# Kernel optimization log

Measured on AMD Instinct MI355X. Metric: run time of the kernel, lower is better.

The kernel has to match this reference:

```python
import jax, jax.numpy as jnp
import numpy as np

N_ITEMS = 512
N_SAMPLES = 32768
WINDOW = 512
CHUNK = WINDOW // 2 + 1          # 257 rfft bins
N_COEFFS = CHUNK * 3             # 771: [mags | phases | start mags]
STEP = WINDOW // 2               # 256 hop
N_FRAMES = N_SAMPLES // STEP     # 128
BASE_RES = 0.5
SPAN = 1.0 - BASE_RES
EPS = 1e-12

_HANN = jnp.asarray(np.hanning(WINDOW), dtype=jnp.float32)


def setup_inputs() -> dict:
    key = jax.random.key(0)
    k1, k2, k3 = jax.random.split(key, 3)
    selections = jax.random.normal(k1, (8, 16, 4, N_ITEMS), dtype=jnp.float32)
    # init(x): uniform(-6, 6) * bernoulli(p=0.01)  -> sparse large-magnitude coeffs
    vals = jax.random.uniform(k2, (N_ITEMS, N_COEFFS), minval=-6.0, maxval=6.0, dtype=jnp.float32)
    mask = (jax.random.uniform(k3, (N_ITEMS, N_COEFFS)) < 0.01).astype(jnp.float32)
    items = vals * mask
    return {"selections": selections, "items": items}


def _resonance_synth(coeffs):
    # coeffs: (B, E, X, N_COEFFS)
    mags = BASE_RES + jax.nn.sigmoid(coeffs[..., :CHUNK]) * 0.9999 * SPAN       # decay per frame, in (0.5, 1)
    phases = jnp.tanh(coeffs[..., CHUNK:2 * CHUNK]) * jnp.pi                    # per-frame phase advance
    starts = jax.nn.sigmoid(coeffs[..., 2 * CHUNK:])                            # initial bin magnitudes

    # log-space cumulative decay scan across frames: mag at frame t = mags ** (t+1)
    t = jnp.arange(1, N_FRAMES + 1, dtype=jnp.float32)                          # (F,)
    log_m = jnp.log(mags + EPS)                                                 # (B,E,X,C)
    decay = jnp.exp(log_m[..., None, :] * t[:, None])                           # (B,E,X,F,C)
    phi = phases[..., None, :] * t[:, None]                                     # cumulative phase rotation

    spec = (starts[..., None, :] * decay).astype(jnp.complex64) * jnp.exp(1j * phi.astype(jnp.complex64))
    frames = jnp.fft.irfft(spec, n=WINDOW, axis=-1).astype(jnp.float32)         # (B,E,X,F,W)
    frames = frames * _HANN

    first = frames[..., :STEP]                                                  # (B,E,X,F,STEP)
    second = frames[..., STEP:]
    shifted = jnp.concatenate([jnp.zeros_like(second[..., :1, :]), second[..., :-1, :]], axis=-2)
    out = first + shifted                                                       # (B,E,X,F,STEP)
    return out.reshape(*frames.shape[:-2], N_FRAMES * STEP)                     # (B,E,X,N_SAMPLES)


def reference(selections, items):
    # select_items with selection_type='relu': non-negative mixture over the item table
    selected = jnp.einsum('bexi,ic->bexc', jax.nn.relu(selections), items)      # (B,E,X,N_COEFFS)
    res = _resonance_synth(selected)                                            # (B,E,X,N_SAMPLES)
    norm = jnp.linalg.norm(res, axis=-1, keepdims=True)
    return res / (norm + 1e-8)                                                  # unit_norm along samples
```

## Files before the change

### kernel.cpp

```cpp
#include <hip/hip_runtime.h>
#include <math.h>

#define N_ROWS   512
#define NBINS    257
#define N_COEFFS 771
#define STEP     256
#define N_FRAMES 128
#define N_SAMP   32768
#define KDIM     576
#define NCHUNK   18
#define PCH      9
#define PCOLS    288
#define TWO_PI   6.283185307179586f
#define PADN     32

typedef _Float16 half8 __attribute__((ext_vector_type(8)));
typedef float floatx4 __attribute__((ext_vector_type(4)));

__global__ __launch_bounds__(256) void k_csc(const float* __restrict__ items,
                                             int* __restrict__ idx,
                                             float* __restrict__ val) {
    int col  = blockIdx.x * 4 + (threadIdx.x >> 6);
    int lane = threadIdx.x & 63;
    if (col >= N_COEFFS) return;
    int base = 0;
    for (int i0 = 0; i0 < 512; i0 += 64) {
        float v = items[(size_t)(i0 + lane) * N_COEFFS + col];
        unsigned long long m = __ballot(v != 0.f);
        int pos = base + __popcll(m & ((1ull << lane) - 1ull));
        if (v != 0.f && pos < PADN) {
            idx[col * PADN + pos] = i0 + lane;
            val[col * PADN + pos] = v;
        }
        base += __popcll(m);
    }
    for (int j = base + lane; j < PADN; j += 64) {
        idx[col * PADN + j] = 0;
        val[col * PADN + j] = 0.f;
    }
}

__global__ __launch_bounds__(256) void k_params(const float* __restrict__ sel,
                                                const int* __restrict__ csc_idx,
                                                const float* __restrict__ csc_val,
                                                float4* __restrict__ pa,
                                                float2* __restrict__ pb) {
    int row = blockIdx.x;
    int tid = threadIdx.x;
    __shared__ float s[512];
    float v0 = sel[row * 512 + tid];
    float v1 = sel[row * 512 + tid + 256];
    s[tid]       = v0 > 0.f ? v0 : 0.f;
    s[tid + 256] = v1 > 0.f ? v1 : 0.f;
    __syncthreads();
    for (int k = tid; k < NBINS; k += 256) {
        float acc[3];
        #pragma unroll
        for (int ch = 0; ch < 3; ++ch) {
            int c = ch * NBINS + k;
            const int*   ip = csc_idx + c * PADN;
            const float* vp = csc_val + c * PADN;
            float a = 0.f;
            #pragma unroll
            for (int j = 0; j < PADN; ++j)
                a = fmaf(s[ip[j]], vp[j], a);
            acc[ch] = a;
        }
        float cm = acc[0], cp = acc[1], cs = acc[2];
        float sig_m = 1.f / (1.f + expf(-cm));
        float mag   = 0.5f + sig_m * 0.9999f * 0.5f;
        float lm    = logf(mag + 1e-12f);
        float ph    = tanhf(cp) * 3.14159265358979323846f;
        float sph, cph;
        sincosf(ph, &sph, &cph);
        float st = 1.f / (1.f + expf(-cs));
        float w  = (k == 0 || k == 256) ? (1.f / 512.f) : (2.f / 512.f);
        int indx = row * NBINS + k;
        pa[indx] = make_float4(lm, ph, cph, sph);
        pb[indx] = make_float2(st * w, mag);
    }
}

__global__ __launch_bounds__(256) void k_basis(_Float16* __restrict__ Bt) {
    int jg  = blockIdx.x;
    int tid = threadIdx.x;
    int n   = ((jg >> 7) << 6) + (jg & 63) + (((jg >> 6) & 1) << 8);
    for (int k = tid; k < KDIM; k += 256) {
        float v = 0.f;
        if (k < NBINS) {
            int r = (k * n) & 511;
            v = cosf(TWO_PI * (float)r * (1.f / 512.f));
        } else if (k < 2 * NBINS) {
            int r = ((k - NBINS) * n) & 511;
            v = -sinf(TWO_PI * (float)r * (1.f / 512.f));
        }
        size_t pos = ((size_t)((k >> 5) * 4 + ((k >> 3) & 3)) * 512 + jg) * 8 + (k & 7);
        Bt[pos] = (_Float16)v;
    }
}

__global__ __launch_bounds__(512, 2) void k_row(const float4* __restrict__ pa,
                                                const float2* __restrict__ pb,
                                                const _Float16* __restrict__ basis,
                                                float* __restrict__ out) {
    __shared__ _Float16 Asm[2][PCH * 4096];
    __shared__ float    SBB[4][64];
    __shared__ float    red[8];

    const int row  = blockIdx.x;
    const int t    = threadIdx.x;
    const int lane = t & 63;
    const int w    = t >> 6;
    const int wm   = w >> 2;
    const int wn   = w & 3;
    const int quad = lane >> 4;
    const int l16  = lane & 15;

    auto agen = [&](int ph) {
        if (t < PCOLS) {
            int gc = ph * PCOLS + t;
            int bin; bool isCos;
            if (gc < NBINS)          { bin = gc;          isCos = true;  }
            else if (gc < 2 * NBINS) { bin = gc - NBINS;  isCos = false; }
            else                     { bin = 0;           isCos = true;  }
            float4 P = pa[row * NBINS + bin];
            float2 Q = pb[row * NBINS + bin];
            float D = 512.f * Q.x * Q.y;
            if (gc >= 2 * NBINS) D = 0.f;
            float c = P.z, s = P.w;
            int ch = t >> 5, g = (t >> 3) & 3, o = t & 7;
            _Float16* base = &Asm[ph][ch * 4096 + o];
            for (int f = 0; f < N_FRAMES; ++f) {
                float val = isCos ? D * c : D * s;
                base[f * 32 + ((g ^ ((f >> 1) & 3) ^ ((f >> 3) & 3)) << 3)] = (_Float16)val;
                D *= Q.y;
                float nc = fmaf(c, P.z, -s * P.w);
                float ns = fmaf(s, P.z,  c * P.w);
                c = nc; s = ns;
            }
        }
    };

    const _Float16* bbase = basis + ((size_t)quad * 512 + wn * 128 + l16) * 8;

    agen(0);
    __syncthreads();

    floatx4 acc[4][8] = {};

    agen(1);
    for (int ks = 0; ks < PCH; ++ks) {
        half8 av[4];
        #pragma unroll
        for (int mt = 0; mt < 4; ++mt) {
            int m = wm * 64 + mt * 16 + l16;
            av[mt] = *(const half8*)&Asm[0][ks * 4096 + m * 32 +
                      ((quad ^ ((m >> 1) & 3) ^ ((m >> 3) & 3)) << 3)];
        }
        const _Float16* bc = bbase + (size_t)ks * 16384;
        #pragma unroll
        for (int nt = 0; nt < 8; ++nt) {
            half8 bv = *(const half8*)(bc + nt * 128);
            #pragma unroll
            for (int mt = 0; mt < 4; ++mt)
                acc[mt][nt] = __builtin_amdgcn_mfma_f32_16x16x32_f16(av[mt], bv, acc[mt][nt], 0, 0, 0);
        }
    }
    __syncthreads();

    for (int ks = 0; ks < PCH; ++ks) {
        half8 av[4];
        #pragma unroll
        for (int mt = 0; mt < 4; ++mt) {
            int m = wm * 64 + mt * 16 + l16;
            av[mt] = *(const half8*)&Asm[1][ks * 4096 + m * 32 +
                      ((quad ^ ((m >> 1) & 3) ^ ((m >> 3) & 3)) << 3)];
        }
        const _Float16* bc = bbase + (size_t)(PCH + ks) * 16384;
        #pragma unroll
        for (int nt = 0; nt < 8; ++nt) {
            half8 bv = *(const half8*)(bc + nt * 128);
            #pragma unroll
            for (int mt = 0; mt < 4; ++mt)
                acc[mt][nt] = __builtin_amdgcn_mfma_f32_16x16x32_f16(av[mt], bv, acc[mt][nt], 0, 0, 0);
        }
    }

    float h1[4], h2[4];
    #pragma unroll
    for (int nt = 0; nt < 4; ++nt) {
        int n1 = wn * 64 + nt * 16 + l16;
        h1[nt] = 0.5f - 0.5f * cosf(TWO_PI * (float)n1 / 511.f);
        h2[nt] = 0.5f - 0.5f * cosf(TWO_PI * (float)(n1 + 256) / 511.f);
    }
    if (wm == 0 && quad == 3) {
        #pragma unroll
        for (int nt = 0; nt < 4; ++nt)
            SBB[wn][nt * 16 + l16] = acc[3][nt + 4][3] * h2[nt];
    }
    __syncthreads();

    float oreg[4][4][4];
    float prevLast[4] = {0.f, 0.f, 0.f, 0.f};
    float ssq = 0.f;
    #pragma unroll
    for (int mt = 0; mt < 4; ++mt) {
        #pragma unroll
        for (int nt = 0; nt < 4; ++nt) {
            float W2[4];
            #pragma unroll
            for (int rr = 0; rr < 4; ++rr) W2[rr] = acc[mt][nt + 4][rr] * h2[nt];
            float tmp = (quad == 3) ? prevLast[nt] : W2[3];
            float carry = __shfl(tmp, (lane + 48) & 63, 64);
            if (mt == 0 && quad == 0)
                carry = (wm == 1) ? SBB[wn][nt * 16 + l16] : 0.f;
            float v = fmaf(acc[mt][nt][0], h1[nt], carry);
            oreg[mt][nt][0] = v; ssq = fmaf(v, v, ssq);
            #pragma unroll
            for (int rr = 1; rr < 4; ++rr) {
                v = fmaf(acc[mt][nt][rr], h1[nt], W2[rr - 1]);
                oreg[mt][nt][rr] = v; ssq = fmaf(v, v, ssq);
            }
            prevLast[nt] = W2[3];
        }
    }

    #pragma unroll
    for (int off = 32; off > 0; off >>= 1) ssq += __shfl_down(ssq, off, 64);
    if (lane == 0) red[w] = ssq;
    __syncthreads();
    float tot = red[0] + red[1] + red[2] + red[3] + red[4] + red[5] + red[6] + red[7];
    float scale = 1.f / (sqrtf(tot) + 1e-8f);

    float* orow = out + (size_t)row * N_SAMP;
    #pragma unroll
    for (int mt = 0; mt < 4; ++mt) {
        #pragma unroll
        for (int nt = 0; nt < 4; ++nt) {
            int n1 = wn * 64 + nt * 16 + l16;
            #pragma unroll
            for (int rr = 0; rr < 4; ++rr) {
                int f = wm * 64 + mt * 16 + quad * 4 + rr;
                orow[f * 256 + n1] = oreg[mt][nt][rr] * scale;
            }
        }
    }
}

extern "C" void kernel_launch(void* const* d_in, const int* in_sizes, int n_in,
                              void* d_out, int out_size, void* d_ws, size_t ws_size,
                              hipStream_t stream) {
    const float* sel   = (const float*)d_in[0];
    const float* items = (const float*)d_in[1];
    float* out = (float*)d_out;

    char* ws = (char*)d_ws;
    size_t off = 0;
    float4* pa   = (float4*)(ws + off); off += (size_t)N_ROWS * NBINS * 16;   off = (off + 255) & ~255ull;
    float2* pb   = (float2*)(ws + off); off += (size_t)N_ROWS * NBINS * 8;    off = (off + 255) & ~255ull;
    _Float16* basis = (_Float16*)(ws + off); off += (size_t)NCHUNK * 4 * 512 * 8 * 2; off = (off + 255) & ~255ull;
    int*   csc_idx = (int*)(ws + off);   off += (size_t)N_COEFFS * PADN * 4;  off = (off + 255) & ~255ull;
    float* csc_val = (float*)(ws + off); off += (size_t)N_COEFFS * PADN * 4;

    k_csc<<<dim3((N_COEFFS + 3) / 4), dim3(256), 0, stream>>>(items, csc_idx, csc_val);
    k_basis<<<dim3(512), dim3(256), 0, stream>>>(basis);
    k_params<<<dim3(N_ROWS), dim3(256), 0, stream>>>(sel, csc_idx, csc_val, pa, pb);
    k_row<<<dim3(N_ROWS), dim3(512), 0, stream>>>(pa, pb, basis, out);
}
```

Before: 167.6 us.

## Coalesce CSC build via shared tile and software-pipeline MFMA operand loads

The sparse-column builder now loads a 64x64 tile of items with coalesced row reads into shared memory and scans columns from there, instead of doing strided per-column global reads. In the main row kernel, the MFMA k-loops double-buffer the A (LDS) and B (global basis) operands in registers, prefetching the next k-step while the current one computes, and precompute the swizzle offsets. This is meant to hide load latency and cut uncoalesced traffic, at the cost of more registers, which may reduce occupancy.

```diff
diff --git a/kernel.cpp b/kernel.cpp
--- a/kernel.cpp
+++ b/kernel.cpp
@@ -20,23 +20,46 @@
 __global__ __launch_bounds__(256) void k_csc(const float* __restrict__ items,
                                              int* __restrict__ idx,
                                              float* __restrict__ val) {
-    int col  = blockIdx.x * 4 + (threadIdx.x >> 6);
-    int lane = threadIdx.x & 63;
-    if (col >= N_COEFFS) return;
-    int base = 0;
-    for (int i0 = 0; i0 < 512; i0 += 64) {
-        float v = items[(size_t)(i0 + lane) * N_COEFFS + col];
-        unsigned long long m = __ballot(v != 0.f);
-        int pos = base + __popcll(m & ((1ull << lane) - 1ull));
-        if (v != 0.f && pos < PADN) {
-            idx[col * PADN + pos] = i0 + lane;
-            val[col * PADN + pos] = v;
-        }
-        base += __popcll(m);
-    }
-    for (int j = base + lane; j < PADN; j += 64) {
-        idx[col * PADN + j] = 0;
-        val[col * PADN + j] = 0.f;
+    __shared__ float tile[64][65];
+    __shared__ int   basec[64];
+    const int c0   = blockIdx.x * 64;
+    const int tid  = threadIdx.x;
+    const int w    = tid >> 6;
+    const int lane = tid & 63;
+    if (tid < 64) basec[tid] = 0;
+    __syncthreads();
+    for (int r0 = 0; r0 < 512; r0 += 64) {
+        #pragma unroll
+        for (int rr = 0; rr < 64; rr += 4) {
+            int r = r0 + rr + w;
+            int c = c0 + lane;
+            float v = (c < N_COEFFS) ? items[(size_t)r * N_COEFFS + c] : 0.f;
+            tile[rr + w][lane] = v;
+        }
+        __syncthreads();
+        for (int cc = 0; cc < 16; ++cc) {
+            int c    = w * 16 + cc;
+            int gcol = c0 + c;
+            float v  = tile[lane][c];
+            unsigned long long m = __ballot(v != 0.f);
+            int base = basec[c];
+            int pos  = base + __popcll(m & ((1ull << lane) - 1ull));
+            if (gcol < N_COEFFS && v != 0.f && pos < PADN) {
+                idx[gcol * PADN + pos] = r0 + lane;
+                val[gcol * PADN + pos] = v;
+            }
+            if (lane == 0) basec[c] = base + __popcll(m);
+        }
+        __syncthreads();
+    }
+    for (int j = tid; j < 64 * PADN; j += 256) {
+        int c = j >> 5, p = j & (PADN - 1);
+        int gcol = c0 + c;
+        int b = basec[c]; b = b < PADN ? b : PADN;
+        if (gcol < N_COEFFS && p >= b) {
+            idx[gcol * PADN + p] = 0;
+            val[gcol * PADN + p] = 0.f;
+        }
     }
 }
 
@@ -142,48 +165,80 @@
     };
 
     const _Float16* bbase = basis + ((size_t)quad * 512 + wn * 128 + l16) * 8;
+    const int aswz[4] = {
+        ((quad ^ (((wm * 64 + 0 * 16 + l16) >> 1) & 3) ^ (((wm * 64 + 0 * 16 + l16) >> 3) & 3)) << 3),
+        ((quad ^ (((wm * 64 + 1 * 16 + l16) >> 1) & 3) ^ (((wm * 64 + 1 * 16 + l16) >> 3) & 3)) << 3),
+        ((quad ^ (((wm * 64 + 2 * 16 + l16) >> 1) & 3) ^ (((wm * 64 + 2 * 16 + l16) >> 3) & 3)) << 3),
+        ((quad ^ (((wm * 64 + 3 * 16 + l16) >> 1) & 3) ^ (((wm * 64 + 3 * 16 + l16) >> 3) & 3)) << 3)
+    };
 
     agen(0);
     __syncthreads();
 
     floatx4 acc[4][8] = {};
-
+    half8 bvC[8], bvN[8], avC[4], avN[4];
+
+    #pragma unroll
+    for (int nt = 0; nt < 8; ++nt) bvC[nt] = *(const half8*)(bbase + nt * 128);
+    #pragma unroll
+    for (int mt = 0; mt < 4; ++mt) {
+        int m = wm * 64 + mt * 16 + l16;
+        avC[mt] = *(const half8*)&Asm[0][m * 32 + aswz[mt]];
+    }
     agen(1);
     for (int ks = 0; ks < PCH; ++ks) {
-        half8 av[4];
+        if (ks + 1 < PCH) {
+            const _Float16* bc = bbase + (size_t)(ks + 1) * 16384;
+            #pragma unroll
+            for (int nt = 0; nt < 8; ++nt) bvN[nt] = *(const half8*)(bc + nt * 128);
+            #pragma unroll
+            for (int mt = 0; mt < 4; ++mt) {
+                int m = wm * 64 + mt * 16 + l16;
+                avN[mt] = *(const half8*)&Asm[0][(ks + 1) * 4096 + m * 32 + aswz[mt]];
+            }
+        }
+        #pragma unroll
+        for (int nt = 0; nt < 8; ++nt)
+            #pragma unroll
+            for (int mt = 0; mt < 4; ++mt)
+                acc[mt][nt] = __builtin_amdgcn_mfma_f32_16x16x32_f16(avC[mt], bvC[nt], acc[mt][nt], 0, 0, 0);
+        #pragma unroll
+        for (int nt = 0; nt < 8; ++nt) bvC[nt] = bvN[nt];
+        #pragma unroll
+        for (int mt = 0; mt < 4; ++mt) avC[mt] = avN[mt];
+    }
+    __syncthreads();
+
+    {
+        const _Float16* bc = bbase + (size_t)PCH * 16384;
+        #pragma unroll
+        for (int nt = 0; nt < 8; ++nt) bvC[nt] = *(const half8*)(bc + nt * 128);
         #pragma unroll
         for (int mt = 0; mt < 4; ++mt) {
             int m = wm * 64 + mt * 16 + l16;
-            av[mt] = *(const half8*)&Asm[0][ks * 4096 + m * 32 +
-                      ((quad ^ ((m >> 1) & 3) ^ ((m >> 3) & 3)) << 3)];
-        }
-        const _Float16* bc = bbase + (size_t)ks * 16384;
-        #pragma unroll
-        for (int nt = 0; nt < 8; ++nt) {
-            half8 bv = *(const half8*)(bc + nt * 128);
+            avC[mt] = *(const half8*)&Asm[1][m * 32 + aswz[mt]];
+        }
+    }
+    for (int ks = 0; ks < PCH; ++ks) {
+        if (ks + 1 < PCH) {
+            const _Float16* bc = bbase + (size_t)(PCH + ks + 1) * 16384;
+            #pragma unroll
+            for (int nt = 0; nt < 8; ++nt) bvN[nt] = *(const half8*)(bc + nt * 128);
+            #pragma unroll
+            for (int mt = 0; mt < 4; ++mt) {
+                int m = wm * 64 + mt * 16 + l16;
+                avN[mt] = *(const half8*)&Asm[1][(ks + 1) * 4096 + m * 32 + aswz[mt]];
+            }
+        }
+        #pragma unroll
+        for (int nt = 0; nt < 8; ++nt)
             #pragma unroll
             for (int mt = 0; mt < 4; ++mt)
-                acc[mt][nt] = __builtin_amdgcn_mfma_f32_16x16x32_f16(av[mt], bv, acc[mt][nt], 0, 0, 0);
-        }
-    }
-    __syncthreads();
-
-    for (int ks = 0; ks < PCH; ++ks) {
-        half8 av[4];
-        #pragma unroll
-        for (int mt = 0; mt < 4; ++mt) {
-            int m = wm * 64 + mt * 16 + l16;
-            av[mt] = *(const half8*)&Asm[1][ks * 4096 + m * 32 +
-                      ((quad ^ ((m >> 1) & 3) ^ ((m >> 3) & 3)) << 3)];
-        }
-        const _Float16* bc = bbase + (size_t)(PCH + ks) * 16384;
-        #pragma unroll
-        for (int nt = 0; nt < 8; ++nt) {
-            half8 bv = *(const half8*)(bc + nt * 128);
-            #pragma unroll
-            for (int mt = 0; mt < 4; ++mt)
-                acc[mt][nt] = __builtin_amdgcn_mfma_f32_16x16x32_f16(av[mt], bv, acc[mt][nt], 0, 0, 0);
-        }
+                acc[mt][nt] = __builtin_amdgcn_mfma_f32_16x16x32_f16(avC[mt], bvC[nt], acc[mt][nt], 0, 0, 0);
+        #pragma unroll
+        for (int nt = 0; nt < 8; ++nt) bvC[nt] = bvN[nt];
+        #pragma unroll
+        for (int mt = 0; mt < 4; ++mt) avC[mt] = avN[mt];
     }
 
     float h1[4], h2[4];
@@ -262,7 +317,7 @@
     int*   csc_idx = (int*)(ws + off);   off += (size_t)N_COEFFS * PADN * 4;  off = (off + 255) & ~255ull;
     float* csc_val = (float*)(ws + off); off += (size_t)N_COEFFS * PADN * 4;
 
-    k_csc<<<dim3((N_COEFFS + 3) / 4), dim3(256), 0, stream>>>(items, csc_idx, csc_val);
+    k_csc<<<dim3((N_COEFFS + 63) / 64), dim3(256), 0, stream>>>(items, csc_idx, csc_val);
     k_basis<<<dim3(512), dim3(256), 0, stream>>>(basis);
     k_params<<<dim3(N_ROWS), dim3(256), 0, stream>>>(sel, csc_idx, csc_val, pa, pb);
     k_row<<<dim3(N_ROWS), dim3(512), 0, stream>>>(pa, pb, basis, out);
```

After: 197.7 us. 18.0% more time.
